# Kernel optimization log

Hardware: AMD Instinct MI355X
Metric: run time of the kernel (lower is better)

The kernel has to match this reference:

```python
import jax, jax.numpy as jnp
import numpy as np

D_MODEL = 768
N_HEADS = 4
N_POINTS = 4
PATCH = 16
IMG = 224
HF = IMG // PATCH  # 14
WF = IMG // PATCH  # 14
LQ = HF * WF       # 196 tokens
DH = D_MODEL // N_HEADS  # 192


def setup_inputs() -> dict:
    key = jax.random.key(0)
    ks = jax.random.split(key, 14)
    s = 0.02
    inp = {
        "x": jax.random.normal(ks[0], (4, 16, 3, IMG, IMG), dtype=jnp.float32),
        # patch-embed conv (Conv2d 3->768, k=16, s=16)
        "embed_w": s * jax.random.normal(ks[1], (D_MODEL, 3, PATCH, PATCH), dtype=jnp.float32),
        "embed_b": jnp.zeros((D_MODEL,), dtype=jnp.float32),
        # MSDeformAttn linears (nn.Linear stores W as [out, in]; y = x @ W.T + b)
        "value_w": s * jax.random.normal(ks[2], (D_MODEL, D_MODEL), dtype=jnp.float32),
        "value_b": jnp.zeros((D_MODEL,), dtype=jnp.float32),
        "off_w": s * jax.random.normal(ks[3], (N_HEADS * N_POINTS * 2, D_MODEL), dtype=jnp.float32),
        "off_b": s * jax.random.normal(ks[4], (N_HEADS * N_POINTS * 2,), dtype=jnp.float32),
        "aw_w": s * jax.random.normal(ks[5], (N_HEADS * N_POINTS, D_MODEL), dtype=jnp.float32),
        "aw_b": jnp.zeros((N_HEADS * N_POINTS,), dtype=jnp.float32),
        "outp_w": s * jax.random.normal(ks[6], (D_MODEL, D_MODEL), dtype=jnp.float32),
        "outp_b": jnp.zeros((D_MODEL,), dtype=jnp.float32),
        # final nn.Linear proj
        "proj_w": s * jax.random.normal(ks[7], (D_MODEL, D_MODEL), dtype=jnp.float32),
        "proj_b": jnp.zeros((D_MODEL,), dtype=jnp.float32),
    }
    return inp


def _patch_embed(x, w, b):
    # x: (N,3,H,W); non-overlapping 16x16 patches == Conv2d(3,D,16,16)
    N = x.shape[0]
    xh = x.reshape(N, 3, HF, PATCH, WF, PATCH)
    feat = jnp.einsum('nchpwq,dcpq->nhwd', xh, w) + b  # (N,HF,WF,D)
    return feat.reshape(N, LQ, D_MODEL)


def _ref_points():
    lin = jnp.linspace(0.0, 1.0, HF)
    gy, gx = jnp.meshgrid(lin, lin, indexing='ij')
    return jnp.stack([gx, gy], -1).reshape(LQ, 2)  # (Lq, 2) in [0,1], (x,y)


def _deform_attn_core(value, loc, attn):
    # value: (N, Lq, M, Dh); loc: (N, Lq, M, P, 2) normalized [0,1]; attn: (N, Lq, M, P)
    N = value.shape[0]
    # grid_sample align_corners=False: pixel = (2*loc-1 + 1)*S/2 - 0.5 = loc*S - 0.5
    px = loc[..., 0] * WF - 0.5
    py = loc[..., 1] * HF - 0.5
    x0 = jnp.floor(px).astype(jnp.int32)
    y0 = jnp.floor(py).astype(jnp.int32)
    x1, y1 = x0 + 1, y0 + 1
    wx1 = px - x0.astype(px.dtype)
    wy1 = py - y0.astype(py.dtype)
    wx0, wy0 = 1.0 - wx1, 1.0 - wy1

    valh = value.transpose(0, 2, 1, 3)  # (N, M, HW, Dh)

    def gather(ix, iy):
        valid = (ix >= 0) & (ix < WF) & (iy >= 0) & (iy < HF)  # zeros padding
        idx = jnp.clip(iy, 0, HF - 1) * WF + jnp.clip(ix, 0, WF - 1)
        idxm = idx.transpose(0, 2, 1, 3).reshape(N, N_HEADS, LQ * N_POINTS)
        g = jnp.take_along_axis(valh, idxm[..., None], axis=2)  # (N,M,Lq*P,Dh)
        g = g * valid.transpose(0, 2, 1, 3).reshape(N, N_HEADS, LQ * N_POINTS, 1)
        return g.reshape(N, N_HEADS, LQ, N_POINTS, DH)

    def w4(a, b):  # (N,Lq,M,P) -> (N,M,Lq,P,1)
        return (a * b).transpose(0, 2, 1, 3)[..., None]

    sampled = (w4(wx0, wy0) * gather(x0, y0) + w4(wx1, wy0) * gather(x1, y0)
               + w4(wx0, wy1) * gather(x0, y1) + w4(wx1, wy1) * gather(x1, y1))
    # weighted combine over points
    out = (sampled * attn.transpose(0, 2, 1, 3)[..., None]).sum(3)  # (N,M,Lq,Dh)
    return out.transpose(0, 2, 1, 3).reshape(N, LQ, D_MODEL)


def reference(x, embed_w, embed_b, value_w, value_b, off_w, off_b, aw_w, aw_b,
              outp_w, outp_b, proj_w, proj_b):
    B, T = x.shape[0], x.shape[1]
    N = B * T
    xi = x.reshape(N, 3, IMG, IMG)
    feat = _patch_embed(xi, embed_w, embed_b)  # (N, Lq, D)

    # MSDeformAttn (n_levels=1)
    value = (feat @ value_w.T + value_b).reshape(N, LQ, N_HEADS, DH)
    off = (feat @ off_w.T + off_b).reshape(N, LQ, N_HEADS, N_POINTS, 2)
    aw = (feat @ aw_w.T + aw_b).reshape(N, LQ, N_HEADS, N_POINTS)
    aw = jax.nn.softmax(aw, axis=-1)  # softmax over n_levels*n_points = 4

    ref = _ref_points()  # (Lq, 2)
    norm = jnp.array([WF, HF], dtype=feat.dtype)  # offset_normalizer = (W, H)
    loc = ref[None, :, None, None, :] + off / norm  # (N,Lq,M,P,2)

    out = _deform_attn_core(value, loc, aw)
    out = out @ outp_w.T + outp_b  # output_proj

    pooled = out.mean(axis=1)  # mean over tokens
    final = pooled @ proj_w.T + proj_b
    return final.reshape(B, T, D_MODEL)
```

## Files before the change

### kernel.cpp

```cpp
#include <hip/hip_runtime.h>
#include <hip/hip_bf16.h>


using bf16 = __bf16;
typedef bf16  bf16x8 __attribute__((ext_vector_type(8)));
typedef float f32x4  __attribute__((ext_vector_type(4)));

#define N_IMG   64
#define LQ      196
#define DM      768
#define NH      4
#define DH      192
#define M_ROWS  (N_IMG * LQ)
#define NCAT    896

#define OFF_A     ((size_t)0)
#define OFF_FEAT  (OFF_A    + 19267584)
#define OFF_WEMB  (OFF_FEAT + 19267584)
#define OFF_WCAT  (OFF_WEMB + 1179648)
#define OFF_BCAT  (OFF_WCAT + 1376256)
#define OFF_VBUF  (OFF_BCAT + 4096)
#define OFF_OA    (OFF_VBUF + 19267584)
#define OFF_CORE  (OFF_OA   + 3211264)
#define OFF_POOL  (OFF_CORE + 196608)

__device__ __forceinline__ void gload_lds16(const bf16* g, bf16* l) {
#if __has_builtin(__builtin_amdgcn_global_load_lds)
  __builtin_amdgcn_global_load_lds(
      (const __attribute__((address_space(1))) void*)g,
      (__attribute__((address_space(3))) void*)l, 16, 0, 0);
#else
  *(bf16x8*)l = *(const bf16x8*)g;
#endif
}

__global__ void stage_kernel(const float* __restrict__ x,
                             const float* __restrict__ embed_w,
                             const float* __restrict__ value_w,
                             const float* __restrict__ off_w,
                             const float* __restrict__ aw_w,
                             const float* __restrict__ value_b,
                             const float* __restrict__ off_b,
                             const float* __restrict__ aw_b,
                             bf16* __restrict__ A,
                             bf16* __restrict__ Wemb, bf16* __restrict__ Wcat,
                             float* __restrict__ bcat, float* __restrict__ core) {
  const int bid = blockIdx.x;
  if (bid < 9408) {
    const int t   = bid * 256 + threadIdx.x;
    const int row = t / 192;
    const int j   = t - row * 192;
    const int k   = j * 4;
    const int c   = k >> 8;
    const int r   = k & 255;
    const int p   = r >> 4;
    const int q   = r & 15;
    const int n   = row / 196;
    const int lq  = row - n * 196;
    const int h   = lq / 14;
    const int w   = lq - h * 14;
    const float4 v = *(const float4*)(x +
        ((((size_t)n * 3 + c) * 224) + h * 16 + p) * 224 + w * 16 + q);
    bf16* dst = A + (size_t)row * DM + k;
    dst[0] = (bf16)v.x; dst[1] = (bf16)v.y; dst[2] = (bf16)v.z; dst[3] = (bf16)v.w;
    return;
  }
  const int idx = (bid - 9408) * 256 + threadIdx.x;
  if (idx < DM * DM) Wemb[idx] = (bf16)embed_w[idx];
  {
    int rr = idx / DM, kk = idx - rr * DM;
    float v = 0.f;
    if (rr < 768)       v = value_w[idx];
    else if (rr < 800)  v = off_w[(rr - 768) * DM + kk];
    else if (rr < 816)  v = aw_w[(rr - 800) * DM + kk];
    Wcat[idx] = (bf16)v;
  }
  if (idx < NCAT) {
    float v = 0.f;
    if (idx < 768)      v = value_b[idx];
    else if (idx < 800) v = off_b[idx - 768];
    else if (idx < 816) v = aw_b[idx - 800];
    bcat[idx] = v;
  }
  if (idx < N_IMG * DM) core[idx] = 0.f;
}

template <typename OutT>
__global__ void gemm_bt(const bf16* __restrict__ A, const bf16* __restrict__ B,
                        const float* __restrict__ bias, OutT* __restrict__ C,
                        int M, int N, int K) {
  __shared__ bf16 As[128 * 64];
  __shared__ bf16 Bs[128 * 64];

  const int tid  = threadIdx.x;
  const int wave = tid >> 6;
  const int lane = tid & 63;
  const int nBase = blockIdx.x * 128;
  const int mBase = blockIdx.y * 128;
  const int wm = wave & 1;
  const int wn = wave >> 1;
  const int quad = lane >> 4;
  const int r16  = lane & 15;

  const f32x4 zero = {0.f, 0.f, 0.f, 0.f};
  f32x4 acc[4][4];
#pragma unroll
  for (int mi = 0; mi < 4; ++mi)
#pragma unroll
    for (int ni = 0; ni < 4; ++ni) acc[mi][ni] = zero;

  const int srow = wave * 32 + (lane >> 3);
  const int scol = (lane & 7) * 8;
  const bf16* Ag = A + (size_t)(mBase + srow) * K + scol;
  const bf16* Bg = B + (size_t)(nBase + srow) * K + scol;
  bf16* Al = As + srow * 64 + scol;
  bf16* Bl = Bs + srow * 64 + scol;

  for (int kt = 0; kt < K; kt += 64) {
#pragma unroll
    for (int i = 0; i < 4; ++i) {
      gload_lds16(Ag + (size_t)(i * 8) * K + kt, Al + i * 8 * 64);
      gload_lds16(Bg + (size_t)(i * 8) * K + kt, Bl + i * 8 * 64);
    }
    __syncthreads();
#pragma unroll
    for (int kk = 0; kk < 64; kk += 32) {
      bf16x8 af[4], bfr[4];
#pragma unroll
      for (int mi = 0; mi < 4; ++mi)
        af[mi] = *(const bf16x8*)&As[(wm * 64 + mi * 16 + r16) * 64 + kk + quad * 8];
#pragma unroll
      for (int ni = 0; ni < 4; ++ni)
        bfr[ni] = *(const bf16x8*)&Bs[(wn * 64 + ni * 16 + r16) * 64 + kk + quad * 8];
#pragma unroll
      for (int mi = 0; mi < 4; ++mi)
#pragma unroll
        for (int ni = 0; ni < 4; ++ni)
          acc[mi][ni] = __builtin_amdgcn_mfma_f32_16x16x32_bf16(
              af[mi], bfr[ni], acc[mi][ni], 0, 0, 0);
    }
    __syncthreads();
  }

#pragma unroll
  for (int ni = 0; ni < 4; ++ni) {
    const int col = nBase + wn * 64 + ni * 16 + r16;
    const float bv = bias[col];
#pragma unroll
    for (int mi = 0; mi < 4; ++mi) {
      const int row0 = mBase + wm * 64 + mi * 16 + quad * 4;
#pragma unroll
      for (int rr = 0; rr < 4; ++rr) {
        float v = acc[mi][ni][rr] + bv;
        C[(size_t)(row0 + rr) * N + col] = (OutT)v;
      }
    }
  }
}

__global__ void gemm2_mixed(const bf16* __restrict__ A, const bf16* __restrict__ B,
                            const float* __restrict__ bias,
                            bf16* __restrict__ Vb, float* __restrict__ OA,
                            int M, int N, int K) {
  __shared__ bf16 As[128 * 64];
  __shared__ bf16 Bs[128 * 64];

  const int tid  = threadIdx.x;
  const int wave = tid >> 6;
  const int lane = tid & 63;
  const int nBase = blockIdx.x * 128;
  const int mBase = blockIdx.y * 128;
  const int wm = wave & 1;
  const int wn = wave >> 1;
  const int quad = lane >> 4;
  const int r16  = lane & 15;

  const f32x4 zero = {0.f, 0.f, 0.f, 0.f};
  f32x4 acc[4][4];
#pragma unroll
  for (int mi = 0; mi < 4; ++mi)
#pragma unroll
    for (int ni = 0; ni < 4; ++ni) acc[mi][ni] = zero;

  const int srow = wave * 32 + (lane >> 3);
  const int scol = (lane & 7) * 8;
  const bf16* Ag = A + (size_t)(mBase + srow) * K + scol;
  const bf16* Bg = B + (size_t)(nBase + srow) * K + scol;
  bf16* Al = As + srow * 64 + scol;
  bf16* Bl = Bs + srow * 64 + scol;

  for (int kt = 0; kt < K; kt += 64) {
#pragma unroll
    for (int i = 0; i < 4; ++i) {
      gload_lds16(Ag + (size_t)(i * 8) * K + kt, Al + i * 8 * 64);
      gload_lds16(Bg + (size_t)(i * 8) * K + kt, Bl + i * 8 * 64);
    }
    __syncthreads();
#pragma unroll
    for (int kk = 0; kk < 64; kk += 32) {
      bf16x8 af[4], bfr[4];
#pragma unroll
      for (int mi = 0; mi < 4; ++mi)
        af[mi] = *(const bf16x8*)&As[(wm * 64 + mi * 16 + r16) * 64 + kk + quad * 8];
#pragma unroll
      for (int ni = 0; ni < 4; ++ni)
        bfr[ni] = *(const bf16x8*)&Bs[(wn * 64 + ni * 16 + r16) * 64 + kk + quad * 8];
#pragma unroll
      for (int mi = 0; mi < 4; ++mi)
#pragma unroll
        for (int ni = 0; ni < 4; ++ni)
          acc[mi][ni] = __builtin_amdgcn_mfma_f32_16x16x32_bf16(
              af[mi], bfr[ni], acc[mi][ni], 0, 0, 0);
    }
    __syncthreads();
  }

#pragma unroll
  for (int ni = 0; ni < 4; ++ni) {
    const int col = nBase + wn * 64 + ni * 16 + r16;
    const float bv = bias[col];
#pragma unroll
    for (int mi = 0; mi < 4; ++mi) {
      const int row0 = mBase + wm * 64 + mi * 16 + quad * 4;
#pragma unroll
      for (int rr = 0; rr < 4; ++rr) {
        float v = acc[mi][ni][rr] + bv;
        int row = row0 + rr;
        if (col < 768) {
          Vb[(size_t)row * 768 + col] = (bf16)v;
        } else if (col < 816) {
          OA[(size_t)row * 64 + (col - 768)] = v;
        }
      }
    }
  }
}

__global__ void deform_kernel(const bf16* __restrict__ Vb,
                              const float* __restrict__ OA,
                              float* __restrict__ core) {
  __shared__ float s_w[64][4];
  __shared__ int   s_t[64][4];

  const int n   = blockIdx.x;
  const int lq0 = blockIdx.y * 4;
  const int z   = blockIdx.z;
  const int tid = threadIdx.x;

  if (tid < 64) {
    const int i = tid >> 4;
    const int m = (tid >> 2) & 3;
    const int p = tid & 3;
    const int lq = lq0 + i;
    const float* row = OA + ((size_t)n * LQ + lq) * 64;

    const float l0 = row[32 + m * 4 + 0];
    const float l1 = row[32 + m * 4 + 1];
    const float l2 = row[32 + m * 4 + 2];
    const float l3 = row[32 + m * 4 + 3];
    const float mx = fmaxf(fmaxf(l0, l1), fmaxf(l2, l3));
    const float e0 = __expf(l0 - mx), e1 = __expf(l1 - mx);
    const float e2 = __expf(l2 - mx), e3 = __expf(l3 - mx);
    const float inv = 1.f / (e0 + e1 + e2 + e3);
    const float ep[4] = {e0, e1, e2, e3};
    const float ew = ep[p] * inv;

    const int h = lq / 14, w = lq - (lq / 14) * 14;
    const float px = (float)w * (14.f / 13.f) - 0.5f + row[(m * 4 + p) * 2 + 0];
    const float py = (float)h * (14.f / 13.f) - 0.5f + row[(m * 4 + p) * 2 + 1];
    const float fx = floorf(px), fy = floorf(py);
    const int x0 = (int)fx, y0 = (int)fy;
    const float wx1 = px - fx, wy1 = py - fy;
    const float wx0 = 1.f - wx1, wy0 = 1.f - wy1;

    const bool vx0 = (x0 >= 0) & (x0 < 14);
    const bool vx1 = (x0 >= -1) & (x0 < 13);
    const bool vy0 = (y0 >= 0) & (y0 < 14);
    const bool vy1 = (y0 >= -1) & (y0 < 13);
    const int cx0 = min(max(x0, 0), 13),      cx1 = min(max(x0 + 1, 0), 13);
    const int cy0 = min(max(y0, 0), 13) * 14, cy1 = min(max(y0 + 1, 0), 13) * 14;

    s_w[tid][0] = (vx0 & vy0) ? ew * wx0 * wy0 : 0.f;
    s_w[tid][1] = (vx1 & vy0) ? ew * wx1 * wy0 : 0.f;
    s_w[tid][2] = (vx0 & vy1) ? ew * wx0 * wy1 : 0.f;
    s_w[tid][3] = (vx1 & vy1) ? ew * wx1 * wy1 : 0.f;
    s_t[tid][0] = cy0 + cx0;
    s_t[tid][1] = cy0 + cx1;
    s_t[tid][2] = cy1 + cx0;
    s_t[tid][3] = cy1 + cx1;
  }
  __syncthreads();

  const int ch = z * 256 + tid;
  const int m  = ch / DH;
  const bf16* vb = Vb + (size_t)n * LQ * 768 + ch;
  float acc = 0.f;
#pragma unroll
  for (int i = 0; i < 4; ++i) {
#pragma unroll
    for (int p = 0; p < 4; ++p) {
      const int e = i * 16 + m * 4 + p;
      const float4 w4 = *(const float4*)s_w[e];
      const int4   t4 = *(const int4*)s_t[e];
      acc += w4.x * (float)vb[(size_t)t4.x * 768];
      acc += w4.y * (float)vb[(size_t)t4.y * 768];
      acc += w4.z * (float)vb[(size_t)t4.z * 768];
      acc += w4.w * (float)vb[(size_t)t4.w * 768];
    }
  }
  atomicAdd(&core[(size_t)n * DM + ch], acc * (1.f / 196.f));
}

__global__ void small_linear(const float* __restrict__ in,
                             const float* __restrict__ W,
                             const float* __restrict__ b,
                             float* __restrict__ out) {
  const int n = blockIdx.x;
  const int d = blockIdx.y * 256 + threadIdx.x;
  const float4* a4 = (const float4*)(in + (size_t)n * DM);
  const float4* w4 = (const float4*)(W + (size_t)d * DM);
  float acc = 0.f;
#pragma unroll 4
  for (int k = 0; k < DM / 4; ++k) {
    float4 a = a4[k], w = w4[k];
    acc += a.x * w.x + a.y * w.y + a.z * w.z + a.w * w.w;
  }
  out[(size_t)n * DM + d] = acc + b[d];
}

extern "C" void kernel_launch(void* const* d_in, const int* in_sizes, int n_in,
                              void* d_out, int out_size, void* d_ws, size_t ws_size,
                              hipStream_t stream) {
  const float* x       = (const float*)d_in[0];
  const float* embed_w = (const float*)d_in[1];
  const float* embed_b = (const float*)d_in[2];
  const float* value_w = (const float*)d_in[3];
  const float* value_b = (const float*)d_in[4];
  const float* off_w   = (const float*)d_in[5];
  const float* off_b   = (const float*)d_in[6];
  const float* aw_w    = (const float*)d_in[7];
  const float* aw_b    = (const float*)d_in[8];
  const float* outp_w  = (const float*)d_in[9];
  const float* outp_b  = (const float*)d_in[10];
  const float* proj_w  = (const float*)d_in[11];
  const float* proj_b  = (const float*)d_in[12];
  float* out = (float*)d_out;

  char* ws = (char*)d_ws;
  bf16*  A      = (bf16*)(ws + OFF_A);
  bf16*  feat   = (bf16*)(ws + OFF_FEAT);
  bf16*  Wemb   = (bf16*)(ws + OFF_WEMB);
  bf16*  Wcat   = (bf16*)(ws + OFF_WCAT);
  float* bcat   = (float*)(ws + OFF_BCAT);
  bf16*  Vbuf   = (bf16*)(ws + OFF_VBUF);
  float* OA     = (float*)(ws + OFF_OA);
  float* core   = (float*)(ws + OFF_CORE);
  float* pooled = (float*)(ws + OFF_POOL);

  stage_kernel<<<dim3(12096), dim3(256), 0, stream>>>(
      x, embed_w, value_w, off_w, aw_w, value_b, off_b, aw_b,
      A, Wemb, Wcat, bcat, core);

  gemm_bt<bf16><<<dim3(DM / 128, M_ROWS / 128), dim3(256), 0, stream>>>(
      A, Wemb, embed_b, feat, M_ROWS, DM, DM);

  gemm2_mixed<<<dim3(NCAT / 128, M_ROWS / 128), dim3(256), 0, stream>>>(
      feat, Wcat, bcat, Vbuf, OA, M_ROWS, NCAT, DM);

  deform_kernel<<<dim3(N_IMG, 49, 3), dim3(256), 0, stream>>>(Vbuf, OA, core);

  small_linear<<<dim3(N_IMG, 3), dim3(256), 0, stream>>>(core, outp_w, outp_b, pooled);
  small_linear<<<dim3(N_IMG, 3), dim3(256), 0, stream>>>(pooled, proj_w, proj_b, out);
}
```

Before: 242.4 us.

## Fold patch-embed weights into value/offset/attn weights, dropping the embed GEMM

Precomputes the product of the value/offset/attention-weight matrices with the patch-embed weight, plus a folded bias, inside the staging kernel. The big im2col activations then feed directly into the single concatenated GEMM, which removes the full 12544x768x768 embed GEMM and its intermediate feature buffer. Weights pass through bf16 twice (product rounded to bf16), which slightly changes numerics. The small pooled linears also now process four images per block with the inputs shared in LDS, so each weight row is reused across images.

```diff
diff --git a/kernel.cpp b/kernel.cpp
--- a/kernel.cpp
+++ b/kernel.cpp
@@ -14,11 +14,15 @@
 #define M_ROWS  (N_IMG * LQ)
 #define NCAT    896
 
+#define B_WGEMM   0
+#define B_BCAT    42
+#define B_ZERO    46
+#define B_IM2COL  94
+#define STAGE_GRID (B_IM2COL + 9408)
+
 #define OFF_A     ((size_t)0)
-#define OFF_FEAT  (OFF_A    + 19267584)
-#define OFF_WEMB  (OFF_FEAT + 19267584)
-#define OFF_WCAT  (OFF_WEMB + 1179648)
-#define OFF_BCAT  (OFF_WCAT + 1376256)
+#define OFF_WC    (OFF_A    + 19267584)
+#define OFF_BCAT  (OFF_WC   + 1376256)
 #define OFF_VBUF  (OFF_BCAT + 4096)
 #define OFF_OA    (OFF_VBUF + 19267584)
 #define OFF_CORE  (OFF_OA   + 3211264)
@@ -36,6 +40,7 @@
 
 __global__ void stage_kernel(const float* __restrict__ x,
                              const float* __restrict__ embed_w,
+                             const float* __restrict__ embed_b,
                              const float* __restrict__ value_w,
                              const float* __restrict__ off_w,
                              const float* __restrict__ aw_w,
@@ -43,11 +48,16 @@
                              const float* __restrict__ off_b,
                              const float* __restrict__ aw_b,
                              bf16* __restrict__ A,
-                             bf16* __restrict__ Wemb, bf16* __restrict__ Wcat,
-                             float* __restrict__ bcat, float* __restrict__ core) {
+                             bf16* __restrict__ Wc,
+                             float* __restrict__ bcat2,
+                             float* __restrict__ core) {
+  __shared__ bf16 As[128 * 64];
+  __shared__ bf16 Bs[128 * 64];
   const int bid = blockIdx.x;
-  if (bid < 9408) {
-    const int t   = bid * 256 + threadIdx.x;
+  const int tid = threadIdx.x;
+
+  if (bid >= B_IM2COL) {
+    const int t   = (bid - B_IM2COL) * 256 + tid;
     const int row = t / 192;
     const int j   = t - row * 192;
     const int k   = j * 4;
@@ -65,97 +75,121 @@
     dst[0] = (bf16)v.x; dst[1] = (bf16)v.y; dst[2] = (bf16)v.z; dst[3] = (bf16)v.w;
     return;
   }
-  const int idx = (bid - 9408) * 256 + threadIdx.x;
-  if (idx < DM * DM) Wemb[idx] = (bf16)embed_w[idx];
-  {
-    int rr = idx / DM, kk = idx - rr * DM;
-    float v = 0.f;
-    if (rr < 768)       v = value_w[idx];
-    else if (rr < 800)  v = off_w[(rr - 768) * DM + kk];
-    else if (rr < 816)  v = aw_w[(rr - 800) * DM + kk];
-    Wcat[idx] = (bf16)v;
-  }
-  if (idx < NCAT) {
-    float v = 0.f;
-    if (idx < 768)      v = value_b[idx];
-    else if (idx < 800) v = off_b[idx - 768];
-    else if (idx < 816) v = aw_b[idx - 800];
-    bcat[idx] = v;
-  }
-  if (idx < N_IMG * DM) core[idx] = 0.f;
-}
-
-template <typename OutT>
-__global__ void gemm_bt(const bf16* __restrict__ A, const bf16* __restrict__ B,
-                        const float* __restrict__ bias, OutT* __restrict__ C,
-                        int M, int N, int K) {
-  __shared__ bf16 As[128 * 64];
-  __shared__ bf16 Bs[128 * 64];
-
-  const int tid  = threadIdx.x;
-  const int wave = tid >> 6;
-  const int lane = tid & 63;
-  const int nBase = blockIdx.x * 128;
-  const int mBase = blockIdx.y * 128;
-  const int wm = wave & 1;
-  const int wn = wave >> 1;
-  const int quad = lane >> 4;
-  const int r16  = lane & 15;
-
-  const f32x4 zero = {0.f, 0.f, 0.f, 0.f};
-  f32x4 acc[4][4];
-#pragma unroll
-  for (int mi = 0; mi < 4; ++mi)
-#pragma unroll
-    for (int ni = 0; ni < 4; ++ni) acc[mi][ni] = zero;
-
-  const int srow = wave * 32 + (lane >> 3);
-  const int scol = (lane & 7) * 8;
-  const bf16* Ag = A + (size_t)(mBase + srow) * K + scol;
-  const bf16* Bg = B + (size_t)(nBase + srow) * K + scol;
-  bf16* Al = As + srow * 64 + scol;
-  bf16* Bl = Bs + srow * 64 + scol;
-
-  for (int kt = 0; kt < K; kt += 64) {
+
+  if (bid < B_BCAT) {
+    const int mT = bid / 6;
+    const int nT = bid - mT * 6;
+    const int oBase = mT * 128;
+    const int nBase = nT * 128;
+    const int wave = tid >> 6;
+    const int lane = tid & 63;
+    const int quad = lane >> 4;
+    const int r16  = lane & 15;
+    const int wm = wave & 1;
+    const int wn = wave >> 1;
+    const int srow = wave * 32 + (lane >> 3);
+    const int scol = (lane & 7) * 8;
+
+    const float* asrc[4];
 #pragma unroll
     for (int i = 0; i < 4; ++i) {
-      gload_lds16(Ag + (size_t)(i * 8) * K + kt, Al + i * 8 * 64);
-      gload_lds16(Bg + (size_t)(i * 8) * K + kt, Bl + i * 8 * 64);
-    }
-    __syncthreads();
-#pragma unroll
-    for (int kk = 0; kk < 64; kk += 32) {
-      bf16x8 af[4], bfr[4];
-#pragma unroll
-      for (int mi = 0; mi < 4; ++mi)
-        af[mi] = *(const bf16x8*)&As[(wm * 64 + mi * 16 + r16) * 64 + kk + quad * 8];
-#pragma unroll
-      for (int ni = 0; ni < 4; ++ni)
-        bfr[ni] = *(const bf16x8*)&Bs[(wn * 64 + ni * 16 + r16) * 64 + kk + quad * 8];
-#pragma unroll
-      for (int mi = 0; mi < 4; ++mi)
+      const int o = oBase + srow + i * 8;
+      asrc[i] = (o < 768) ? value_w + (size_t)o * DM
+              : (o < 800) ? off_w + (size_t)(o - 768) * DM
+              : (o < 816) ? aw_w + (size_t)(o - 800) * DM : nullptr;
+    }
+
+    const f32x4 zero = {0.f, 0.f, 0.f, 0.f};
+    f32x4 acc[4][4];
+#pragma unroll
+    for (int mi = 0; mi < 4; ++mi)
+#pragma unroll
+      for (int ni = 0; ni < 4; ++ni) acc[mi][ni] = zero;
+
+    for (int kt = 0; kt < DM; kt += 64) {
+#pragma unroll
+      for (int i = 0; i < 4; ++i) {
+        const int r = srow + i * 8;
+        bf16x8 av;
+        if (asrc[i]) {
+          const float4 f0 = *(const float4*)(asrc[i] + kt + scol);
+          const float4 f1 = *(const float4*)(asrc[i] + kt + scol + 4);
+          av[0] = (bf16)f0.x; av[1] = (bf16)f0.y;
+          av[2] = (bf16)f0.z; av[3] = (bf16)f0.w;
+          av[4] = (bf16)f1.x; av[5] = (bf16)f1.y;
+          av[6] = (bf16)f1.z; av[7] = (bf16)f1.w;
+        } else {
+#pragma unroll
+          for (int jj = 0; jj < 8; ++jj) av[jj] = (bf16)0.f;
+        }
+        *(bf16x8*)&As[r * 64 + scol] = av;
+        const int n = nBase + r;
+        bf16x8 bv;
+#pragma unroll
+        for (int jj = 0; jj < 8; ++jj)
+          bv[jj] = (bf16)embed_w[(size_t)(kt + scol + jj) * DM + n];
+        *(bf16x8*)&Bs[r * 64 + scol] = bv;
+      }
+      __syncthreads();
+#pragma unroll
+      for (int kk = 0; kk < 64; kk += 32) {
+        bf16x8 af[4], bfr[4];
+#pragma unroll
+        for (int mi = 0; mi < 4; ++mi)
+          af[mi] = *(const bf16x8*)&As[(wm * 64 + mi * 16 + r16) * 64 + kk + quad * 8];
 #pragma unroll
         for (int ni = 0; ni < 4; ++ni)
-          acc[mi][ni] = __builtin_amdgcn_mfma_f32_16x16x32_bf16(
-              af[mi], bfr[ni], acc[mi][ni], 0, 0, 0);
-    }
-    __syncthreads();
-  }
-
-#pragma unroll
-  for (int ni = 0; ni < 4; ++ni) {
-    const int col = nBase + wn * 64 + ni * 16 + r16;
-    const float bv = bias[col];
-#pragma unroll
-    for (int mi = 0; mi < 4; ++mi) {
-      const int row0 = mBase + wm * 64 + mi * 16 + quad * 4;
-#pragma unroll
-      for (int rr = 0; rr < 4; ++rr) {
-        float v = acc[mi][ni][rr] + bv;
-        C[(size_t)(row0 + rr) * N + col] = (OutT)v;
+          bfr[ni] = *(const bf16x8*)&Bs[(wn * 64 + ni * 16 + r16) * 64 + kk + quad * 8];
+#pragma unroll
+        for (int mi = 0; mi < 4; ++mi)
+#pragma unroll
+          for (int ni = 0; ni < 4; ++ni)
+            acc[mi][ni] = __builtin_amdgcn_mfma_f32_16x16x32_bf16(
+                af[mi], bfr[ni], acc[mi][ni], 0, 0, 0);
       }
-    }
-  }
+      __syncthreads();
+    }
+#pragma unroll
+    for (int ni = 0; ni < 4; ++ni) {
+      const int col = nBase + wn * 64 + ni * 16 + r16;
+#pragma unroll
+      for (int mi = 0; mi < 4; ++mi) {
+        const int row0 = oBase + wm * 64 + mi * 16 + quad * 4;
+#pragma unroll
+        for (int rr = 0; rr < 4; ++rr)
+          Wc[(size_t)(row0 + rr) * DM + col] = (bf16)acc[mi][ni][rr];
+      }
+    }
+    return;
+  }
+
+  if (bid < B_ZERO) {
+    const int o = (bid - B_BCAT) * 256 + tid;
+    if (o < NCAT) {
+      float bias_o = (o < 768) ? value_b[o]
+                   : (o < 800) ? off_b[o - 768]
+                   : (o < 816) ? aw_b[o - 800] : 0.f;
+      float acc = 0.f;
+      if (o < 816) {
+        const float* wr = (o < 768) ? value_w + (size_t)o * DM
+                        : (o < 800) ? off_w + (size_t)(o - 768) * DM
+                        : aw_w + (size_t)(o - 800) * DM;
+        const float4* w4p = (const float4*)wr;
+        const float4* b4p = (const float4*)embed_b;
+#pragma unroll 4
+        for (int k = 0; k < DM / 4; ++k) {
+          const float4 wv = w4p[k], bv = b4p[k];
+          acc += wv.x * bv.x + wv.y * bv.y + wv.z * bv.z + wv.w * bv.w;
+        }
+      }
+      bcat2[o] = acc + bias_o;
+    }
+    return;
+  }
+
+  const int i = (bid - B_ZERO) * 256 + tid;
+  f32x4 z = {0.f, 0.f, 0.f, 0.f};
+  ((f32x4*)core)[i] = z;
 }
 
 __global__ void gemm2_mixed(const bf16* __restrict__ A, const bf16* __restrict__ B,
@@ -311,21 +345,40 @@
   atomicAdd(&core[(size_t)n * DM + ch], acc * (1.f / 196.f));
 }
 
-__global__ void small_linear(const float* __restrict__ in,
-                             const float* __restrict__ W,
-                             const float* __restrict__ b,
-                             float* __restrict__ out) {
-  const int n = blockIdx.x;
-  const int d = blockIdx.y * 256 + threadIdx.x;
-  const float4* a4 = (const float4*)(in + (size_t)n * DM);
-  const float4* w4 = (const float4*)(W + (size_t)d * DM);
-  float acc = 0.f;
+__global__ void small_linear4(const float* __restrict__ in,
+                              const float* __restrict__ W,
+                              const float* __restrict__ b,
+                              float* __restrict__ out) {
+  __shared__ float s_in[4 * DM];
+  const int tid = threadIdx.x;
+  const int n0 = blockIdx.x * 4;
+  const float4* src = (const float4*)(in + (size_t)n0 * DM);
+#pragma unroll
+  for (int i = 0; i < 3; ++i)
+    ((float4*)s_in)[tid + i * 256] = src[tid + i * 256];
+  __syncthreads();
+
+  const int d = blockIdx.y * 256 + tid;
+  const float4* w4p = (const float4*)(W + (size_t)d * DM);
+  const float4* s0 = (const float4*)(s_in);
+  const float4* s1 = (const float4*)(s_in + DM);
+  const float4* s2 = (const float4*)(s_in + 2 * DM);
+  const float4* s3 = (const float4*)(s_in + 3 * DM);
+  float a0 = 0.f, a1 = 0.f, a2 = 0.f, a3 = 0.f;
 #pragma unroll 4
   for (int k = 0; k < DM / 4; ++k) {
-    float4 a = a4[k], w = w4[k];
-    acc += a.x * w.x + a.y * w.y + a.z * w.z + a.w * w.w;
-  }
-  out[(size_t)n * DM + d] = acc + b[d];
+    const float4 w = w4p[k];
+    const float4 v0 = s0[k], v1 = s1[k], v2 = s2[k], v3 = s3[k];
+    a0 += w.x * v0.x + w.y * v0.y + w.z * v0.z + w.w * v0.w;
+    a1 += w.x * v1.x + w.y * v1.y + w.z * v1.z + w.w * v1.w;
+    a2 += w.x * v2.x + w.y * v2.y + w.z * v2.z + w.w * v2.w;
+    a3 += w.x * v3.x + w.y * v3.y + w.z * v3.z + w.w * v3.w;
+  }
+  const float bv = b[d];
+  out[(size_t)(n0 + 0) * DM + d] = a0 + bv;
+  out[(size_t)(n0 + 1) * DM + d] = a1 + bv;
+  out[(size_t)(n0 + 2) * DM + d] = a2 + bv;
+  out[(size_t)(n0 + 3) * DM + d] = a3 + bv;
 }
 
 extern "C" void kernel_launch(void* const* d_in, const int* in_sizes, int n_in,
@@ -348,27 +401,22 @@
 
   char* ws = (char*)d_ws;
   bf16*  A      = (bf16*)(ws + OFF_A);
-  bf16*  feat   = (bf16*)(ws + OFF_FEAT);
-  bf16*  Wemb   = (bf16*)(ws + OFF_WEMB);
-  bf16*  Wcat   = (bf16*)(ws + OFF_WCAT);
-  float* bcat   = (float*)(ws + OFF_BCAT);
+  bf16*  Wc     = (bf16*)(ws + OFF_WC);
+  float* bcat2  = (float*)(ws + OFF_BCAT);
   bf16*  Vbuf   = (bf16*)(ws + OFF_VBUF);
   float* OA     = (float*)(ws + OFF_OA);
   float* core   = (float*)(ws + OFF_CORE);
   float* pooled = (float*)(ws + OFF_POOL);
 
-  stage_kernel<<<dim3(12096), dim3(256), 0, stream>>>(
-      x, embed_w, value_w, off_w, aw_w, value_b, off_b, aw_b,
-      A, Wemb, Wcat, bcat, core);
-
-  gemm_bt<bf16><<<dim3(DM / 128, M_ROWS / 128), dim3(256), 0, stream>>>(
-      A, Wemb, embed_b, feat, M_ROWS, DM, DM);
+  stage_kernel<<<dim3(STAGE_GRID), dim3(256), 0, stream>>>(
+      x, embed_w, embed_b, value_w, off_w, aw_w, value_b, off_b, aw_b,
+      A, Wc, bcat2, core);
 
   gemm2_mixed<<<dim3(NCAT / 128, M_ROWS / 128), dim3(256), 0, stream>>>(
-      feat, Wcat, bcat, Vbuf, OA, M_ROWS, NCAT, DM);
+      A, Wc, bcat2, Vbuf, OA, M_ROWS, NCAT, DM);
 
   deform_kernel<<<dim3(N_IMG, 49, 3), dim3(256), 0, stream>>>(Vbuf, OA, core);
 
-  small_linear<<<dim3(N_IMG, 3), dim3(256), 0, stream>>>(core, outp_w, outp_b, pooled);
-  small_linear<<<dim3(N_IMG, 3), dim3(256), 0, stream>>>(pooled, proj_w, proj_b, out);
-}
+  small_linear4<<<dim3(N_IMG / 4, 3), dim3(256), 0, stream>>>(core, outp_w, outp_b, pooled);
+  small_linear4<<<dim3(N_IMG / 4, 3), dim3(256), 0, stream>>>(pooled, proj_w, proj_b, out);
+}
```

Measured after the change: 279.7 us. +15.4%, slower.
